# Kernel optimization log

Measured on AMD Instinct MI355X. Metric: run time of the kernel, lower is better.

## Reference

```python
import jax, jax.numpy as jnp
import numpy as np

B, S, D, OUT = 4, 4096, 256, 64
SCALE = 1.0 / np.sqrt(64.0)  # module hard-codes / 64**0.5


def setup_inputs() -> dict:
    key = jax.random.key(0)
    k1, k2 = jax.random.split(key)
    x = jax.random.normal(k1, (B, S, D), dtype=jnp.float32)
    kernel = jax.random.normal(k2, (3, D, OUT), dtype=jnp.float32) * 0.05
    return {"x": x, "kernel": kernel}


def reference(x, kernel):
    # Single-head attention with shared-input Q/K/V projections.
    q = jnp.einsum('bsd,do->bso', x, kernel[0])
    k = jnp.einsum('bsd,do->bso', x, kernel[1])
    v = jnp.einsum('bsd,do->bso', x, kernel[2])
    scores = jnp.einsum('bqo,bko->bqk', q, k) * SCALE  # [B,S,S]
    attn = jax.nn.softmax(scores, axis=-1)
    return jnp.einsum('bqk,bko->bqo', attn, v)  # [B,S,OUT]
```

## Files before the change

kernel.cpp:

```cpp
#include <hip/hip_runtime.h>

#define SLEN 4096
#define NB 4
#define DIN 256
#define DOUT 64
#define KVSPLIT 2
#define KVBLK 64
#define QBLK 64
#define NT ((SLEN / KVSPLIT) / KVBLK)

typedef _Float16 f16;
typedef _Float16 f16x8 __attribute__((ext_vector_type(8)));
typedef _Float16 f16x4 __attribute__((ext_vector_type(4)));
typedef float f32x4 __attribute__((ext_vector_type(4)));

#define LOG2E 1.4426950408889634f
#define PSHIFT 3.0f

#define GLD16(gsrc, ldst)                                          \
  __builtin_amdgcn_global_load_lds(                                \
      (const __attribute__((address_space(1))) void*)(gsrc),       \
      (__attribute__((address_space(3))) void*)(ldst), 16, 0, 0)

__global__ __launch_bounds__(256) void wt_kernel(
    const float* __restrict__ w, f16* __restrict__ wth) {
  for (int idx = blockIdx.x * 256 + threadIdx.x; idx < 3 * DIN * DOUT;
       idx += gridDim.x * 256) {
    int m = idx / (DIN * DOUT);
    int r = idx - m * (DIN * DOUT);
    int k = r >> 6, o = r & 63;
    wth[(m * DOUT + o) * DIN + k] = (f16)w[idx];
  }
}

__global__ __launch_bounds__(64) void proj_kernel(
    const float* __restrict__ x, const f16* __restrict__ wth,
    f16* __restrict__ qh, f16* __restrict__ kh, f16* __restrict__ vth) {
  __shared__ alignas(16) f16 vbuf[16 * 64];
  const int lane = threadIdx.x;
  const int c = lane & 15, g = lane >> 4;
  const int tb = blockIdx.x * 16;
  const int b = tb >> 12, s0 = tb & 4095;

  f16x8 a[8];
  {
    const float* xr = x + (size_t)(tb + c) * DIN + g * 8;
#pragma unroll
    for (int ks = 0; ks < 8; ++ks) {
      f32x4 lo = *(const f32x4*)(xr + ks * 32);
      f32x4 hi = *(const f32x4*)(xr + ks * 32 + 4);
      f16x8 av;
#pragma unroll
      for (int j = 0; j < 4; ++j) { av[j] = (f16)lo[j]; av[j + 4] = (f16)hi[j]; }
      a[ks] = av;
    }
  }

#pragma unroll
  for (int m = 0; m < 3; ++m) {
    const f16* wb = wth + (size_t)m * DOUT * DIN + (size_t)c * DIN + g * 8;
    f32x4 acc[4];
#pragma unroll
    for (int nt = 0; nt < 4; ++nt) acc[nt] = (f32x4){0.f, 0.f, 0.f, 0.f};
#pragma unroll
    for (int ks = 0; ks < 8; ++ks)
#pragma unroll
      for (int nt = 0; nt < 4; ++nt) {
        f16x8 bf = *(const f16x8*)(wb + (size_t)(nt * 16) * DIN + ks * 32);
        acc[nt] = __builtin_amdgcn_mfma_f32_16x16x32_f16(a[ks], bf, acc[nt], 0, 0, 0);
      }

    if (m < 2) {
#pragma unroll
      for (int nt = 0; nt < 4; ++nt)
#pragma unroll
        for (int rr = 0; rr < 4; ++rr) {
          int row = tb + g * 4 + rr;
          int o = nt * 16 + c;
          float v = acc[nt][rr];
          if (m == 0)
            qh[(size_t)row * DOUT + o] = (f16)(v * 0.125f);
          else
            kh[(size_t)row * DOUT + o] = (f16)v;
        }
    } else {
#pragma unroll
      for (int nt = 0; nt < 4; ++nt)
#pragma unroll
        for (int rr = 0; rr < 4; ++rr) {
          int sl = 4 * g + rr;
          vbuf[sl * 64 + ((nt * 16 + c) ^ ((sl & 7) << 3))] = (f16)acc[nt][rr];
        }
      f16x8 r0, r1;
#pragma unroll
      for (int s = 0; s < 8; ++s) r0[s] = vbuf[s * 64 + (lane ^ ((s & 7) << 3))];
#pragma unroll
      for (int s = 8; s < 16; ++s) r1[s - 8] = vbuf[s * 64 + (lane ^ ((s & 7) << 3))];
      f16* dst = vth + ((size_t)b * DOUT + lane) * SLEN + s0;
      *(f16x8*)(dst) = r0;
      *(f16x8*)(dst + 8) = r1;
    }
  }
}

__global__ __launch_bounds__(256, 4) void attn_kernel(
    const f16* __restrict__ qh, const f16* __restrict__ kh,
    const f16* __restrict__ vth, float* __restrict__ pO,
    float* __restrict__ pL) {
  __shared__ alignas(16) f16 kb[2][KVBLK * 64];
  __shared__ alignas(16) f16 vb[2][KVBLK * 64];
  __shared__ alignas(16) f16 pbuf[4][16 * 64];

  const int tid = threadIdx.x;
  const int lane = tid & 63;
  const int c = lane & 15, g = lane >> 4;
  const int wv = tid >> 6;

  const int wg = ((blockIdx.x & 7) << 6) + (blockIdx.x >> 3);
  const int b = wg >> 7;
  const int split = (wg >> 6) & 1;
  const int qb = wg & 63;
  const int q0 = qb * QBLK + wv * 16;
  const int kv0 = split * (SLEN / KVSPLIT);

  f16* plds = pbuf[wv];

  const int srow = tid >> 3;
  const int scol = (tid & 7) * 8;
  const f16* kgbase = kh + (size_t)b * SLEN * DOUT;
  const f16* vgbase = vth + (size_t)b * DOUT * SLEN;

  f16x8 qf[2];
  {
    const f16* qr = qh + ((size_t)(b * SLEN + q0 + c)) * DOUT + g * 8;
    qf[0] = *(const f16x8*)(qr);
    qf[1] = *(const f16x8*)(qr + 32);
  }

  f32x4 oacc[4];
#pragma unroll
  for (int nt = 0; nt < 4; ++nt) oacc[nt] = (f32x4){0.f, 0.f, 0.f, 0.f};
  float lrun = 0.f;

  auto stage = [&](int sel, int kv) {
#pragma unroll
    for (int rr = 0; rr < 2; ++rr) {
      int r = srow + rr * 32;
      int sw = scol ^ ((r & 7) << 3);
      GLD16(kgbase + (size_t)(kv + r) * DOUT + sw,
            (char*)(&kb[sel][0]) + wv * 1024 + rr * 4096);
      GLD16(vgbase + (size_t)r * SLEN + kv + sw,
            (char*)(&vb[sel][0]) + wv * 1024 + rr * 4096);
    }
  };

  stage(0, kv0);
  __syncthreads();

  for (int t = 0; t < NT; ++t) {
    const int sel = t & 1;
    if (t + 1 < NT) stage(sel ^ 1, kv0 + (t + 1) * KVBLK);

    f32x4 sacc[4];
#pragma unroll
    for (int t4 = 0; t4 < 4; ++t4) {
      sacc[t4] = (f32x4){0.f, 0.f, 0.f, 0.f};
      f16x8 k0 = *(const f16x8*)&kb[sel][(16 * t4 + c) * 64 + 8 * (g ^ (c & 7))];
      f16x8 k1 = *(const f16x8*)&kb[sel][(16 * t4 + c) * 64 + 8 * ((g + 4) ^ (c & 7))];
      sacc[t4] = __builtin_amdgcn_mfma_f32_16x16x32_f16(k0, qf[0], sacc[t4], 0, 0, 0);
      sacc[t4] = __builtin_amdgcn_mfma_f32_16x16x32_f16(k1, qf[1], sacc[t4], 0, 0, 0);
    }

    f16x4 pk[4];
#pragma unroll
    for (int t4 = 0; t4 < 4; ++t4)
#pragma unroll
      for (int r = 0; r < 4; ++r) {
        float p = exp2f(fmaf(sacc[t4][r], LOG2E, -PSHIFT * LOG2E));
        lrun += p;
        pk[t4][r] = (f16)p;
      }

#pragma unroll
    for (int t4 = 0; t4 < 4; ++t4)
      *(f16x4*)&plds[c * 64 + ((16 * t4 + 4 * g) ^ ((c & 7) << 3))] = pk[t4];

#pragma unroll
    for (int s2 = 0; s2 < 2; ++s2) {
      f16x8 pa = *(const f16x8*)&plds[c * 64 + ((s2 * 32 + g * 8) ^ ((c & 7) << 3))];
#pragma unroll
      for (int nt = 0; nt < 4; ++nt) {
        f16x8 vf = *(const f16x8*)&vb[sel][(16 * nt + c) * 64 + 8 * ((g + 4 * s2) ^ (c & 7))];
        oacc[nt] = __builtin_amdgcn_mfma_f32_16x16x32_f16(pa, vf, oacc[nt], 0, 0, 0);
      }
    }

    __syncthreads();
  }

  const size_t rowb = (size_t)b * SLEN + q0;
  float* po = pO + ((size_t)split * (NB * SLEN) + rowb) * DOUT;
#pragma unroll
  for (int nt = 0; nt < 4; ++nt)
#pragma unroll
    for (int r = 0; r < 4; ++r)
      po[(size_t)(4 * g + r) * DOUT + nt * 16 + c] = oacc[nt][r];
  lrun += __shfl_xor(lrun, 16);
  lrun += __shfl_xor(lrun, 32);
  if (lane < 16) pL[(size_t)split * (NB * SLEN) + rowb + lane] = lrun;
}

__global__ __launch_bounds__(256) void combine_kernel(
    const float* __restrict__ pO, const float* __restrict__ pL,
    float* __restrict__ out) {
  int i = blockIdx.x * 256 + threadIdx.x;
  int row = i >> 4;
  int c4 = (i & 15) * 4;
  f32x4 a = (f32x4){0.f, 0.f, 0.f, 0.f};
  float L = 0.f;
#pragma unroll
  for (int s = 0; s < KVSPLIT; ++s) {
    a += *(const f32x4*)&pO[((size_t)s * (NB * SLEN) + row) * DOUT + c4];
    L += pL[(size_t)s * (NB * SLEN) + row];
  }
  float rl = 1.0f / L;
  f32x4 o = a * rl;
  *(f32x4*)&out[(size_t)row * DOUT + c4] = o;
}

extern "C" void kernel_launch(void* const* d_in, const int* in_sizes, int n_in,
                              void* d_out, int out_size, void* d_ws, size_t ws_size,
                              hipStream_t stream) {
  const float* x = (const float*)d_in[0];
  const float* w = (const float*)d_in[1];
  float* out = (float*)d_out;

  const size_t NE = (size_t)NB * SLEN * DOUT;
  f16* qh = (f16*)d_ws;
  f16* kh = qh + NE;
  f16* vth = kh + NE;
  f16* wth = vth + NE;
  float* pO = (float*)(wth + 3 * DIN * DOUT);
  float* pL = pO + (size_t)KVSPLIT * NE;

  hipLaunchKernelGGL(wt_kernel, dim3(12), dim3(256), 0, stream, w, wth);
  hipLaunchKernelGGL(proj_kernel, dim3(NB * SLEN / 16), dim3(64), 0, stream,
                     x, wth, qh, kh, vth);
  hipLaunchKernelGGL(attn_kernel, dim3(NB * KVSPLIT * (SLEN / QBLK)), dim3(256),
                     0, stream, qh, kh, vth, pO, pL);
  hipLaunchKernelGGL(combine_kernel, dim3(NB * SLEN * DOUT / 4 / 256), dim3(256),
                     0, stream, pO, pL, out);
}
```

Baseline: 132.7 us.

## Split KV four ways with atomic accumulation, split projection grid, fold log2e into Q

Raises the KV split from 2 to 4 so more workgroups run, and accumulates partial outputs and row sums into the output buffer with float atomics, replacing the combine kernel with an in-place normalization. The projection kernel gets a grid dimension per Q/K/V matrix and stages its outputs through LDS so global stores are coalesced. log2(e) and the softmax scale are folded into Q, which saves an FMA per score, and s_setprio is raised around the MFMA sections. The costs are two memsets, atomic contention on the output, nondeterministic summation order, and recomputing the x-to-fp16 conversion once per matrix.

Measured after the change: 130.7 us. About the same (-1.5%).

```diff
diff --git a/kernel.cpp b/kernel.cpp
--- a/kernel.cpp
+++ b/kernel.cpp
@@ -4,7 +4,7 @@
 #define NB 4
 #define DIN 256
 #define DOUT 64
-#define KVSPLIT 2
+#define KVSPLIT 4
 #define KVBLK 64
 #define QBLK 64
 #define NT ((SLEN / KVSPLIT) / KVBLK)
@@ -14,8 +14,8 @@
 typedef _Float16 f16x4 __attribute__((ext_vector_type(4)));
 typedef float f32x4 __attribute__((ext_vector_type(4)));
 
-#define LOG2E 1.4426950408889634f
-#define PSHIFT 3.0f
+#define QSCALE 0.1803368801111204f
+#define PSHIFT2 4.328085122666891f
 
 #define GLD16(gsrc, ldst)                                          \
   __builtin_amdgcn_global_load_lds(                                \
@@ -36,9 +36,10 @@
 __global__ __launch_bounds__(64) void proj_kernel(
     const float* __restrict__ x, const f16* __restrict__ wth,
     f16* __restrict__ qh, f16* __restrict__ kh, f16* __restrict__ vth) {
-  __shared__ alignas(16) f16 vbuf[16 * 64];
+  __shared__ alignas(16) f16 tbuf[64 * 24];
   const int lane = threadIdx.x;
   const int c = lane & 15, g = lane >> 4;
+  const int m = blockIdx.y;
   const int tb = blockIdx.x * 16;
   const int b = tb >> 12, s0 = tb & 4095;
 
@@ -56,56 +57,48 @@
     }
   }
 
-#pragma unroll
-  for (int m = 0; m < 3; ++m) {
-    const f16* wb = wth + (size_t)m * DOUT * DIN + (size_t)c * DIN + g * 8;
-    f32x4 acc[4];
-#pragma unroll
-    for (int nt = 0; nt < 4; ++nt) acc[nt] = (f32x4){0.f, 0.f, 0.f, 0.f};
-#pragma unroll
-    for (int ks = 0; ks < 8; ++ks)
-#pragma unroll
-      for (int nt = 0; nt < 4; ++nt) {
-        f16x8 bf = *(const f16x8*)(wb + (size_t)(nt * 16) * DIN + ks * 32);
-        acc[nt] = __builtin_amdgcn_mfma_f32_16x16x32_f16(a[ks], bf, acc[nt], 0, 0, 0);
-      }
-
-    if (m < 2) {
-#pragma unroll
-      for (int nt = 0; nt < 4; ++nt)
-#pragma unroll
-        for (int rr = 0; rr < 4; ++rr) {
-          int row = tb + g * 4 + rr;
-          int o = nt * 16 + c;
-          float v = acc[nt][rr];
-          if (m == 0)
-            qh[(size_t)row * DOUT + o] = (f16)(v * 0.125f);
-          else
-            kh[(size_t)row * DOUT + o] = (f16)v;
-        }
-    } else {
-#pragma unroll
-      for (int nt = 0; nt < 4; ++nt)
-#pragma unroll
-        for (int rr = 0; rr < 4; ++rr) {
-          int sl = 4 * g + rr;
-          vbuf[sl * 64 + ((nt * 16 + c) ^ ((sl & 7) << 3))] = (f16)acc[nt][rr];
-        }
-      f16x8 r0, r1;
-#pragma unroll
-      for (int s = 0; s < 8; ++s) r0[s] = vbuf[s * 64 + (lane ^ ((s & 7) << 3))];
-#pragma unroll
-      for (int s = 8; s < 16; ++s) r1[s - 8] = vbuf[s * 64 + (lane ^ ((s & 7) << 3))];
-      f16* dst = vth + ((size_t)b * DOUT + lane) * SLEN + s0;
-      *(f16x8*)(dst) = r0;
-      *(f16x8*)(dst + 8) = r1;
-    }
+  const f16* wb = wth + (size_t)m * DOUT * DIN + (size_t)c * DIN + g * 8;
+  f32x4 acc[4];
+#pragma unroll
+  for (int nt = 0; nt < 4; ++nt) acc[nt] = (f32x4){0.f, 0.f, 0.f, 0.f};
+#pragma unroll
+  for (int ks = 0; ks < 8; ++ks)
+#pragma unroll
+    for (int nt = 0; nt < 4; ++nt) {
+      f16x8 bf = *(const f16x8*)(wb + (size_t)(nt * 16) * DIN + ks * 32);
+      acc[nt] = __builtin_amdgcn_mfma_f32_16x16x32_f16(a[ks], bf, acc[nt], 0, 0, 0);
+    }
+
+  if (m < 2) {
+#pragma unroll
+    for (int nt = 0; nt < 4; ++nt)
+#pragma unroll
+      for (int rr = 0; rr < 4; ++rr)
+        tbuf[(4 * g + rr) * 72 + nt * 16 + c] =
+            (f16)(m == 0 ? acc[nt][rr] * QSCALE : acc[nt][rr]);
+    const int rw = lane >> 2, cb = (lane & 3) * 16;
+    f16x8 r0 = *(const f16x8*)&tbuf[rw * 72 + cb];
+    f16x8 r1 = *(const f16x8*)&tbuf[rw * 72 + cb + 8];
+    f16* dst = (m == 0 ? qh : kh) + (size_t)(tb + rw) * DOUT + cb;
+    *(f16x8*)(dst) = r0;
+    *(f16x8*)(dst + 8) = r1;
+  } else {
+#pragma unroll
+    for (int nt = 0; nt < 4; ++nt)
+#pragma unroll
+      for (int rr = 0; rr < 4; ++rr)
+        tbuf[(nt * 16 + c) * 24 + 4 * g + rr] = (f16)acc[nt][rr];
+    f16x8 r0 = *(const f16x8*)&tbuf[lane * 24];
+    f16x8 r1 = *(const f16x8*)&tbuf[lane * 24 + 8];
+    f16* dst = vth + ((size_t)b * DOUT + lane) * SLEN + s0;
+    *(f16x8*)(dst) = r0;
+    *(f16x8*)(dst + 8) = r1;
   }
 }
 
 __global__ __launch_bounds__(256, 4) void attn_kernel(
     const f16* __restrict__ qh, const f16* __restrict__ kh,
-    const f16* __restrict__ vth, float* __restrict__ pO,
+    const f16* __restrict__ vth, float* __restrict__ out,
     float* __restrict__ pL) {
   __shared__ alignas(16) f16 kb[2][KVBLK * 64];
   __shared__ alignas(16) f16 vb[2][KVBLK * 64];
@@ -116,9 +109,9 @@
   const int c = lane & 15, g = lane >> 4;
   const int wv = tid >> 6;
 
-  const int wg = ((blockIdx.x & 7) << 6) + (blockIdx.x >> 3);
-  const int b = wg >> 7;
-  const int split = (wg >> 6) & 1;
+  const int wg = ((blockIdx.x & 7) << 7) + (blockIdx.x >> 3);
+  const int b = wg >> 8;
+  const int split = (wg >> 6) & 3;
   const int qb = wg & 63;
   const int q0 = qb * QBLK + wv * 16;
   const int kv0 = split * (SLEN / KVSPLIT);
@@ -162,6 +155,7 @@
     if (t + 1 < NT) stage(sel ^ 1, kv0 + (t + 1) * KVBLK);
 
     f32x4 sacc[4];
+    __builtin_amdgcn_s_setprio(1);
 #pragma unroll
     for (int t4 = 0; t4 < 4; ++t4) {
       sacc[t4] = (f32x4){0.f, 0.f, 0.f, 0.f};
@@ -170,13 +164,14 @@
       sacc[t4] = __builtin_amdgcn_mfma_f32_16x16x32_f16(k0, qf[0], sacc[t4], 0, 0, 0);
       sacc[t4] = __builtin_amdgcn_mfma_f32_16x16x32_f16(k1, qf[1], sacc[t4], 0, 0, 0);
     }
+    __builtin_amdgcn_s_setprio(0);
 
     f16x4 pk[4];
 #pragma unroll
     for (int t4 = 0; t4 < 4; ++t4)
 #pragma unroll
       for (int r = 0; r < 4; ++r) {
-        float p = exp2f(fmaf(sacc[t4][r], LOG2E, -PSHIFT * LOG2E));
+        float p = exp2f(sacc[t4][r] - PSHIFT2);
         lrun += p;
         pk[t4][r] = (f16)p;
       }
@@ -185,6 +180,7 @@
     for (int t4 = 0; t4 < 4; ++t4)
       *(f16x4*)&plds[c * 64 + ((16 * t4 + 4 * g) ^ ((c & 7) << 3))] = pk[t4];
 
+    __builtin_amdgcn_s_setprio(1);
 #pragma unroll
     for (int s2 = 0; s2 < 2; ++s2) {
       f16x8 pa = *(const f16x8*)&plds[c * 64 + ((s2 * 32 + g * 8) ^ ((c & 7) << 3))];
@@ -194,38 +190,31 @@
         oacc[nt] = __builtin_amdgcn_mfma_f32_16x16x32_f16(pa, vf, oacc[nt], 0, 0, 0);
       }
     }
+    __builtin_amdgcn_s_setprio(0);
 
     __syncthreads();
   }
 
   const size_t rowb = (size_t)b * SLEN + q0;
-  float* po = pO + ((size_t)split * (NB * SLEN) + rowb) * DOUT;
+  float* po = out + rowb * DOUT;
 #pragma unroll
   for (int nt = 0; nt < 4; ++nt)
 #pragma unroll
     for (int r = 0; r < 4; ++r)
-      po[(size_t)(4 * g + r) * DOUT + nt * 16 + c] = oacc[nt][r];
+      atomicAdd(&po[(size_t)(4 * g + r) * DOUT + nt * 16 + c], oacc[nt][r]);
   lrun += __shfl_xor(lrun, 16);
   lrun += __shfl_xor(lrun, 32);
-  if (lane < 16) pL[(size_t)split * (NB * SLEN) + rowb + lane] = lrun;
-}
-
-__global__ __launch_bounds__(256) void combine_kernel(
-    const float* __restrict__ pO, const float* __restrict__ pL,
-    float* __restrict__ out) {
+  if (lane < 16) atomicAdd(&pL[rowb + lane], lrun);
+}
+
+__global__ __launch_bounds__(256) void norm_kernel(
+    float* __restrict__ out, const float* __restrict__ pL) {
   int i = blockIdx.x * 256 + threadIdx.x;
   int row = i >> 4;
-  int c4 = (i & 15) * 4;
-  f32x4 a = (f32x4){0.f, 0.f, 0.f, 0.f};
-  float L = 0.f;
-#pragma unroll
-  for (int s = 0; s < KVSPLIT; ++s) {
-    a += *(const f32x4*)&pO[((size_t)s * (NB * SLEN) + row) * DOUT + c4];
-    L += pL[(size_t)s * (NB * SLEN) + row];
-  }
-  float rl = 1.0f / L;
-  f32x4 o = a * rl;
-  *(f32x4*)&out[(size_t)row * DOUT + c4] = o;
+  float rl = 1.0f / pL[row];
+  f32x4 o = *(const f32x4*)&out[(size_t)i * 4];
+  o *= rl;
+  *(f32x4*)&out[(size_t)i * 4] = o;
 }
 
 extern "C" void kernel_launch(void* const* d_in, const int* in_sizes, int n_in,
@@ -240,14 +229,15 @@
   f16* kh = qh + NE;
   f16* vth = kh + NE;
   f16* wth = vth + NE;
-  float* pO = (float*)(wth + 3 * DIN * DOUT);
-  float* pL = pO + (size_t)KVSPLIT * NE;
-
+  float* pL = (float*)(wth + 3 * DIN * DOUT);
+
+  hipMemsetAsync(out, 0, NE * sizeof(float), stream);
+  hipMemsetAsync(pL, 0, (size_t)NB * SLEN * sizeof(float), stream);
   hipLaunchKernelGGL(wt_kernel, dim3(12), dim3(256), 0, stream, w, wth);
-  hipLaunchKernelGGL(proj_kernel, dim3(NB * SLEN / 16), dim3(64), 0, stream,
+  hipLaunchKernelGGL(proj_kernel, dim3(NB * SLEN / 16, 3), dim3(64), 0, stream,
                      x, wth, qh, kh, vth);
   hipLaunchKernelGGL(attn_kernel, dim3(NB * KVSPLIT * (SLEN / QBLK)), dim3(256),
-                     0, stream, qh, kh, vth, pO, pL);
-  hipLaunchKernelGGL(combine_kernel, dim3(NB * SLEN * DOUT / 4 / 256), dim3(256),
-                     0, stream, pO, pL, out);
-}
+                     0, stream, qh, kh, vth, out, pL);
+  hipLaunchKernelGGL(norm_kernel, dim3(NB * SLEN * DOUT / 4 / 256), dim3(256),
+                     0, stream, out, pL);
+}
```
